# Kernel optimization log

Hardware: AMD Instinct MI355X
Metric: run time of the kernel (lower is better)

The kernel has to match this reference:

```python
import jax, jax.numpy as jnp
import numpy as np

N_POINTS = 131072
N_SEG = 16
C = 256
BN_EPS = 1e-5


def setup_inputs() -> dict:
    key = jax.random.key(0)
    ks = jax.random.split(key, 6)
    x = jax.random.normal(ks[0], (N_POINTS, C), jnp.float32)
    # Ragged segment end-offsets (cumulative counts), strictly increasing, last == N_POINTS.
    rng = np.random.default_rng(0)
    base = N_POINTS // N_SEG
    counts = base + rng.integers(-base // 32, base // 32, N_SEG)
    counts[-1] += N_POINTS - counts.sum()
    o = jnp.asarray(np.cumsum(counts), jnp.int32)
    s1 = 1.0 / np.sqrt(2 * C)  # linear1: Linear(2C -> C)
    s2 = 1.0 / np.sqrt(C)      # linear2: Linear(C -> C)
    W1 = jax.random.uniform(ks[1], (2 * C, C), jnp.float32, -s1, s1)
    b1 = jax.random.uniform(ks[2], (C,), jnp.float32, -s1, s1)
    W2 = jax.random.uniform(ks[3], (C, C), jnp.float32, -s2, s2)
    b2 = jax.random.uniform(ks[4], (C,), jnp.float32, -s2, s2)
    gamma = jnp.ones((C,), jnp.float32)
    beta = jnp.zeros((C,), jnp.float32)
    return {"x": x, "o": o, "W1": W1, "b1": b1, "W2": W2, "b2": b2,
            "gamma": gamma, "beta": beta}


def reference(x, o, W1, b1, W2, b2, gamma, beta):
    n, c = x.shape
    s = o.shape[0]
    # segment id per point from cumulative end-offsets
    seg_id = jnp.searchsorted(o, jnp.arange(n), side="right")  # [N]
    counts = jnp.concatenate([o[:1], o[1:] - o[:-1]])          # [S]
    # per-segment mean pooling (x_b.sum(0, True) / cnt)
    sums = jax.ops.segment_sum(x, seg_id, num_segments=s)      # [S, C]
    means = sums / counts[:, None].astype(x.dtype)
    # linear2: Linear(C, C) + ReLU on segment means
    y = jax.nn.relu(means @ W2 + b2)                           # [S, C]
    # broadcast-concat back to points, then linear1: Linear(2C, C)
    h = jnp.concatenate([x, y[seg_id]], axis=1) @ W1 + b1      # [N, C]
    # BatchNorm1d (training mode: batch statistics, biased variance) + ReLU
    mu = h.mean(axis=0)
    var = h.var(axis=0)
    out = jax.nn.relu((h - mu) * (gamma / jnp.sqrt(var + BN_EPS)) + beta)
    return out
```

## Files before the change

### kernel.cpp

```cpp
#include <hip/hip_runtime.h>
#include <hip/hip_bf16.h>
#include <stdint.h>

#define N_PTS 131072
#define NC 256
#define NSEG 16
#define BN_EPSF 1e-5f

typedef __attribute__((ext_vector_type(8))) short bf16x8;
typedef __attribute__((ext_vector_type(4))) float f32x4;

__device__ __forceinline__ unsigned short f2bf(float f) {
  union { float f; uint32_t u; } v; v.f = f;
  uint32_t u = v.u;
  uint32_t r = (u + 0x7fffu + ((u >> 16) & 1u)) >> 16;
  return (unsigned short)r;
}
__device__ __forceinline__ float bf2f(unsigned short h) {
  union { uint32_t u; float f; } v; v.u = ((uint32_t)h) << 16; return v.f;
}

__global__ void k_zero(float* __restrict__ p, int n) {
  int i = blockIdx.x * 256 + threadIdx.x;
  if (i < n) p[i] = 0.f;
}

__global__ __launch_bounds__(256) void k_segsum_convert(
    const float* __restrict__ x, const int* __restrict__ o,
    unsigned short* __restrict__ x_bf, float* __restrict__ seg_sums) {
  __shared__ int o_s[NSEG];
  int t = threadIdx.x;
  if (t < NSEG) o_s[t] = o[t];
  __syncthreads();
  int g = t >> 6, l = t & 63;
  int row0 = blockIdx.x * 128;
  int c0 = l * 4;
  int cur = 0;
  {
    int rf = row0 + g;
    while (o_s[cur] <= rf) ++cur;
  }
  float4 acc = {0.f, 0.f, 0.f, 0.f};
  const float4* xv = (const float4*)x;
  for (int i = 0; i < 32; ++i) {
    int r = row0 + g + i * 4;
    if (r >= o_s[cur]) {
      atomicAdd(&seg_sums[cur * NC + c0 + 0], acc.x);
      atomicAdd(&seg_sums[cur * NC + c0 + 1], acc.y);
      atomicAdd(&seg_sums[cur * NC + c0 + 2], acc.z);
      atomicAdd(&seg_sums[cur * NC + c0 + 3], acc.w);
      acc.x = acc.y = acc.z = acc.w = 0.f;
      do { ++cur; } while (o_s[cur] <= r);
    }
    float4 v = xv[r * 64 + l];
    ushort4 b;
    b.x = f2bf(v.x); b.y = f2bf(v.y); b.z = f2bf(v.z); b.w = f2bf(v.w);
    *(ushort4*)(x_bf + r * NC + c0) = b;
    acc.x += v.x; acc.y += v.y; acc.z += v.z; acc.w += v.w;
  }
  atomicAdd(&seg_sums[cur * NC + c0 + 0], acc.x);
  atomicAdd(&seg_sums[cur * NC + c0 + 1], acc.y);
  atomicAdd(&seg_sums[cur * NC + c0 + 2], acc.z);
  atomicAdd(&seg_sums[cur * NC + c0 + 3], acc.w);
}

__global__ void k_w1t(const float* __restrict__ W1, unsigned short* __restrict__ w1t) {
  int j = blockIdx.x, k = threadIdx.x;
  w1t[j * NC + k] = f2bf(W1[k * NC + j]);
}

__global__ __launch_bounds__(256) void k_seg_mlp(
    const int* __restrict__ o, const float* __restrict__ seg_sums,
    const float* __restrict__ W1, const float* __restrict__ b1,
    const float* __restrict__ W2, const float* __restrict__ b2,
    float* __restrict__ z) {
  __shared__ float mean_s[NC];
  __shared__ float y_s[NC];
  int b = blockIdx.x, j = threadIdx.x;
  int start = (b == 0) ? 0 : o[b - 1];
  float inv = 1.f / (float)(o[b] - start);
  mean_s[j] = seg_sums[b * NC + j] * inv;
  __syncthreads();
  float a = b2[j];
  for (int k = 0; k < NC; ++k) a += mean_s[k] * W2[k * NC + j];
  y_s[j] = fmaxf(a, 0.f);
  __syncthreads();
  float a2 = b1[j];
  for (int k = 0; k < NC; ++k) a2 += y_s[k] * W1[(NC + k) * NC + j];
  z[b * NC + j] = a2;
}

__global__ __launch_bounds__(256) void k_gemm(
    const unsigned short* __restrict__ x_bf, const unsigned short* __restrict__ w1t,
    const int* __restrict__ o, const float* __restrict__ z,
    unsigned short* __restrict__ h_bf,
    float* __restrict__ colsum, float* __restrict__ colsumsq) {
  __shared__ __align__(16) unsigned short lA[128 * 32];
  __shared__ __align__(16) unsigned short lB[128 * 32];
  __shared__ float s_sum[128];
  __shared__ float s_sq[128];
  __shared__ int o_s[NSEG];

  int t = threadIdx.x;
  int lane = t & 63, w = t >> 6;
  int wr = w >> 1, wc = w & 1;
  int bid = blockIdx.x;
  int ct = bid & 1, rt = bid >> 1;
  const int row0 = rt * 128, colT = ct * 128;

  if (t < 128) { s_sum[t] = 0.f; s_sq[t] = 0.f; }
  if (t < NSEG) o_s[t] = o[t];

  f32x4 acc[4][4] = {};

  for (int kt = 0; kt < 8; ++kt) {
    {
      int c = t;
      const unsigned short* ga = x_bf + (size_t)(row0 + (c >> 2)) * NC + kt * 32 + (c & 3) * 8;
      __builtin_amdgcn_global_load_lds(
          (const __attribute__((address_space(1))) void*)ga,
          (__attribute__((address_space(3))) void*)(lA + c * 8), 16, 0, 0);
      const unsigned short* gb = w1t + (size_t)(colT + (c >> 2)) * NC + kt * 32 + (c & 3) * 8;
      __builtin_amdgcn_global_load_lds(
          (const __attribute__((address_space(1))) void*)gb,
          (__attribute__((address_space(3))) void*)(lB + c * 8), 16, 0, 0);
      c = t + 256;
      ga = x_bf + (size_t)(row0 + (c >> 2)) * NC + kt * 32 + (c & 3) * 8;
      __builtin_amdgcn_global_load_lds(
          (const __attribute__((address_space(1))) void*)ga,
          (__attribute__((address_space(3))) void*)(lA + c * 8), 16, 0, 0);
      gb = w1t + (size_t)(colT + (c >> 2)) * NC + kt * 32 + (c & 3) * 8;
      __builtin_amdgcn_global_load_lds(
          (const __attribute__((address_space(1))) void*)gb,
          (__attribute__((address_space(3))) void*)(lB + c * 8), 16, 0, 0);
    }
    __syncthreads();
    bf16x8 af[4], bf[4];
#pragma unroll
    for (int m = 0; m < 4; ++m)
      af[m] = *(const bf16x8*)(lA + (wr * 64 + m * 16 + (lane & 15)) * 32 + (lane >> 4) * 8);
#pragma unroll
    for (int n = 0; n < 4; ++n)
      bf[n] = *(const bf16x8*)(lB + (wc * 64 + n * 16 + (lane & 15)) * 32 + (lane >> 4) * 8);
#pragma unroll
    for (int m = 0; m < 4; ++m)
#pragma unroll
      for (int n = 0; n < 4; ++n)
        acc[m][n] = __builtin_amdgcn_mfma_f32_16x16x32_bf16(af[m], bf[n], acc[m][n], 0, 0, 0);
    __syncthreads();
  }

  int s0 = 0;
  while (o_s[s0] <= row0) ++s0;
  int e0 = o_s[s0];
  int s1 = (s0 < NSEG - 1) ? s0 + 1 : s0;
  int cl = lane & 15, q = lane >> 4;
#pragma unroll
  for (int n = 0; n < 4; ++n) {
    int col = colT + wc * 64 + n * 16 + cl;
    float zA = z[s0 * NC + col], zB = z[s1 * NC + col];
    float ps = 0.f, pq = 0.f;
#pragma unroll
    for (int m = 0; m < 4; ++m) {
      int rbase = row0 + wr * 64 + m * 16 + q * 4;
#pragma unroll
      for (int r = 0; r < 4; ++r) {
        int row = rbase + r;
        float hv = acc[m][n][r] + ((row < e0) ? zA : zB);
        h_bf[(size_t)row * NC + col] = f2bf(hv);
        ps += hv; pq += hv * hv;
      }
    }
    ps += __shfl_xor(ps, 16, 64); ps += __shfl_xor(ps, 32, 64);
    pq += __shfl_xor(pq, 16, 64); pq += __shfl_xor(pq, 32, 64);
    if (q == 0) {
      atomicAdd(&s_sum[wc * 64 + n * 16 + cl], ps);
      atomicAdd(&s_sq[wc * 64 + n * 16 + cl], pq);
    }
  }
  __syncthreads();
  if (t < 128) {
    atomicAdd(&colsum[colT + t], s_sum[t]);
    atomicAdd(&colsumsq[colT + t], s_sq[t]);
  }
}

__global__ void k_bn_final(const float* __restrict__ colsum, const float* __restrict__ colsumsq,
                           const float* __restrict__ gamma, const float* __restrict__ beta,
                           float* __restrict__ scale, float* __restrict__ shift) {
  int t = threadIdx.x;
  float invN = 1.f / (float)N_PTS;
  float mu = colsum[t] * invN;
  float var = colsumsq[t] * invN - mu * mu;
  float sc = gamma[t] * rsqrtf(var + BN_EPSF);
  scale[t] = sc;
  shift[t] = beta[t] - mu * sc;
}

__global__ __launch_bounds__(256) void k_bn_apply(
    const unsigned short* __restrict__ h_bf, const float* __restrict__ scale,
    const float* __restrict__ shift, float* __restrict__ out) {
  __shared__ float s_sc[NC];
  __shared__ float s_sh[NC];
  int t = threadIdx.x;
  s_sc[t] = scale[t];
  s_sh[t] = shift[t];
  __syncthreads();
  size_t idx = (size_t)blockIdx.x * 256 + t;
  size_t l0 = idx * 8;
  int col = (int)(l0 & 255);
  uint4 hv = *(const uint4*)(h_bf + l0);
  float f0 = bf2f((unsigned short)(hv.x & 0xffffu));
  float f1 = bf2f((unsigned short)(hv.x >> 16));
  float f2 = bf2f((unsigned short)(hv.y & 0xffffu));
  float f3 = bf2f((unsigned short)(hv.y >> 16));
  float f4 = bf2f((unsigned short)(hv.z & 0xffffu));
  float f5 = bf2f((unsigned short)(hv.z >> 16));
  float f6 = bf2f((unsigned short)(hv.w & 0xffffu));
  float f7 = bf2f((unsigned short)(hv.w >> 16));
  float4 o0, o1;
  o0.x = fmaxf(f0 * s_sc[col + 0] + s_sh[col + 0], 0.f);
  o0.y = fmaxf(f1 * s_sc[col + 1] + s_sh[col + 1], 0.f);
  o0.z = fmaxf(f2 * s_sc[col + 2] + s_sh[col + 2], 0.f);
  o0.w = fmaxf(f3 * s_sc[col + 3] + s_sh[col + 3], 0.f);
  o1.x = fmaxf(f4 * s_sc[col + 4] + s_sh[col + 4], 0.f);
  o1.y = fmaxf(f5 * s_sc[col + 5] + s_sh[col + 5], 0.f);
  o1.z = fmaxf(f6 * s_sc[col + 6] + s_sh[col + 6], 0.f);
  o1.w = fmaxf(f7 * s_sc[col + 7] + s_sh[col + 7], 0.f);
  *(float4*)(out + l0) = o0;
  *(float4*)(out + l0 + 4) = o1;
}

extern "C" void kernel_launch(void* const* d_in, const int* in_sizes, int n_in,
                              void* d_out, int out_size, void* d_ws, size_t ws_size,
                              hipStream_t stream) {
  const float* x = (const float*)d_in[0];
  const int* o = (const int*)d_in[1];
  const float* W1 = (const float*)d_in[2];
  const float* b1 = (const float*)d_in[3];
  const float* W2 = (const float*)d_in[4];
  const float* b2 = (const float*)d_in[5];
  const float* gamma = (const float*)d_in[6];
  const float* beta = (const float*)d_in[7];
  float* out = (float*)d_out;

  char* ws = (char*)d_ws;
  unsigned short* x_bf = (unsigned short*)ws;
  unsigned short* h_bf = (unsigned short*)(ws + 67108864);
  char* base2 = ws + 134217728;
  float* seg_sums = (float*)(base2);
  float* colsum   = (float*)(base2 + 16384);
  float* colsumsq = (float*)(base2 + 17408);
  float* z        = (float*)(base2 + 18432);
  float* scale    = (float*)(base2 + 34816);
  float* shift    = (float*)(base2 + 35840);
  unsigned short* w1t = (unsigned short*)(base2 + 36864);

  k_zero<<<18, 256, 0, stream>>>(seg_sums, 4608);
  k_segsum_convert<<<1024, 256, 0, stream>>>(x, o, x_bf, seg_sums);
  k_w1t<<<256, 256, 0, stream>>>(W1, w1t);
  k_seg_mlp<<<16, 256, 0, stream>>>(o, seg_sums, W1, b1, W2, b2, z);
  k_gemm<<<2048, 256, 0, stream>>>(x_bf, w1t, o, z, h_bf, colsum, colsumsq);
  k_bn_final<<<1, 256, 0, stream>>>(colsum, colsumsq, gamma, beta, scale, shift);
  k_bn_apply<<<16384, 256, 0, stream>>>(h_bf, scale, shift, out);
}
```

Measured before the change: 380.4 us.

## Reduce segment sums in shared memory, tile W1 transpose, narrow bn_apply per thread

```diff
diff --git a/kernel.cpp b/kernel.cpp
--- a/kernel.cpp
+++ b/kernel.cpp
@@ -29,44 +29,65 @@
     const float* __restrict__ x, const int* __restrict__ o,
     unsigned short* __restrict__ x_bf, float* __restrict__ seg_sums) {
   __shared__ int o_s[NSEG];
+  __shared__ float s_acc[2][NC];
   int t = threadIdx.x;
   if (t < NSEG) o_s[t] = o[t];
+  s_acc[0][t] = 0.f;
+  s_acc[1][t] = 0.f;
   __syncthreads();
   int g = t >> 6, l = t & 63;
-  int row0 = blockIdx.x * 128;
+  int row0 = blockIdx.x * 64;
   int c0 = l * 4;
-  int cur = 0;
-  {
-    int rf = row0 + g;
-    while (o_s[cur] <= rf) ++cur;
-  }
-  float4 acc = {0.f, 0.f, 0.f, 0.f};
+  int s0 = 0;
+  while (o_s[s0] <= row0) ++s0;
+  int e0 = o_s[s0];
+  int s1 = (s0 < NSEG - 1) ? s0 + 1 : s0;
+  float4 accA = {0.f, 0.f, 0.f, 0.f}, accB = {0.f, 0.f, 0.f, 0.f};
   const float4* xv = (const float4*)x;
-  for (int i = 0; i < 32; ++i) {
+#pragma unroll
+  for (int i = 0; i < 16; ++i) {
     int r = row0 + g + i * 4;
-    if (r >= o_s[cur]) {
-      atomicAdd(&seg_sums[cur * NC + c0 + 0], acc.x);
-      atomicAdd(&seg_sums[cur * NC + c0 + 1], acc.y);
-      atomicAdd(&seg_sums[cur * NC + c0 + 2], acc.z);
-      atomicAdd(&seg_sums[cur * NC + c0 + 3], acc.w);
-      acc.x = acc.y = acc.z = acc.w = 0.f;
-      do { ++cur; } while (o_s[cur] <= r);
-    }
-    float4 v = xv[r * 64 + l];
+    float4 v = xv[(size_t)r * 64 + l];
     ushort4 b;
     b.x = f2bf(v.x); b.y = f2bf(v.y); b.z = f2bf(v.z); b.w = f2bf(v.w);
-    *(ushort4*)(x_bf + r * NC + c0) = b;
-    acc.x += v.x; acc.y += v.y; acc.z += v.z; acc.w += v.w;
-  }
-  atomicAdd(&seg_sums[cur * NC + c0 + 0], acc.x);
-  atomicAdd(&seg_sums[cur * NC + c0 + 1], acc.y);
-  atomicAdd(&seg_sums[cur * NC + c0 + 2], acc.z);
-  atomicAdd(&seg_sums[cur * NC + c0 + 3], acc.w);
-}
-
-__global__ void k_w1t(const float* __restrict__ W1, unsigned short* __restrict__ w1t) {
-  int j = blockIdx.x, k = threadIdx.x;
-  w1t[j * NC + k] = f2bf(W1[k * NC + j]);
+    *(ushort4*)(x_bf + (size_t)r * NC + c0) = b;
+    bool inA = (r < e0);
+    accA.x += inA ? v.x : 0.f; accB.x += inA ? 0.f : v.x;
+    accA.y += inA ? v.y : 0.f; accB.y += inA ? 0.f : v.y;
+    accA.z += inA ? v.z : 0.f; accB.z += inA ? 0.f : v.z;
+    accA.w += inA ? v.w : 0.f; accB.w += inA ? 0.f : v.w;
+  }
+  atomicAdd(&s_acc[0][c0 + 0], accA.x);
+  atomicAdd(&s_acc[0][c0 + 1], accA.y);
+  atomicAdd(&s_acc[0][c0 + 2], accA.z);
+  atomicAdd(&s_acc[0][c0 + 3], accA.w);
+  atomicAdd(&s_acc[1][c0 + 0], accB.x);
+  atomicAdd(&s_acc[1][c0 + 1], accB.y);
+  atomicAdd(&s_acc[1][c0 + 2], accB.z);
+  atomicAdd(&s_acc[1][c0 + 3], accB.w);
+  __syncthreads();
+  atomicAdd(&seg_sums[s0 * NC + t], s_acc[0][t]);
+  atomicAdd(&seg_sums[s1 * NC + t], s_acc[1][t]);
+}
+
+__global__ __launch_bounds__(256) void k_w1t(const float* __restrict__ W1,
+                                             unsigned short* __restrict__ w1t) {
+  __shared__ float tile[64][65];
+  int t = threadIdx.x;
+  int bx = blockIdx.x & 3, by = blockIdx.x >> 2;
+  int k0 = by * 64, j0 = bx * 64;
+  int r = t >> 6, c = t & 63;
+#pragma unroll
+  for (int i = 0; i < 16; ++i) {
+    int kk = r + i * 4;
+    tile[kk][c] = W1[(size_t)(k0 + kk) * NC + j0 + c];
+  }
+  __syncthreads();
+#pragma unroll
+  for (int i = 0; i < 16; ++i) {
+    int jj = r + i * 4;
+    w1t[(size_t)(j0 + jj) * NC + k0 + c] = f2bf(tile[c][jj]);
+  }
 }
 
 __global__ __launch_bounds__(256) void k_seg_mlp(
@@ -200,35 +221,23 @@
 __global__ __launch_bounds__(256) void k_bn_apply(
     const unsigned short* __restrict__ h_bf, const float* __restrict__ scale,
     const float* __restrict__ shift, float* __restrict__ out) {
-  __shared__ float s_sc[NC];
-  __shared__ float s_sh[NC];
-  int t = threadIdx.x;
-  s_sc[t] = scale[t];
-  s_sh[t] = shift[t];
-  __syncthreads();
+  int t = threadIdx.x;
   size_t idx = (size_t)blockIdx.x * 256 + t;
-  size_t l0 = idx * 8;
+  size_t l0 = idx * 4;
   int col = (int)(l0 & 255);
-  uint4 hv = *(const uint4*)(h_bf + l0);
+  uint2 hv = *(const uint2*)(h_bf + l0);
+  float4 sc = *(const float4*)(scale + col);
+  float4 sh = *(const float4*)(shift + col);
   float f0 = bf2f((unsigned short)(hv.x & 0xffffu));
   float f1 = bf2f((unsigned short)(hv.x >> 16));
   float f2 = bf2f((unsigned short)(hv.y & 0xffffu));
   float f3 = bf2f((unsigned short)(hv.y >> 16));
-  float f4 = bf2f((unsigned short)(hv.z & 0xffffu));
-  float f5 = bf2f((unsigned short)(hv.z >> 16));
-  float f6 = bf2f((unsigned short)(hv.w & 0xffffu));
-  float f7 = bf2f((unsigned short)(hv.w >> 16));
-  float4 o0, o1;
-  o0.x = fmaxf(f0 * s_sc[col + 0] + s_sh[col + 0], 0.f);
-  o0.y = fmaxf(f1 * s_sc[col + 1] + s_sh[col + 1], 0.f);
-  o0.z = fmaxf(f2 * s_sc[col + 2] + s_sh[col + 2], 0.f);
-  o0.w = fmaxf(f3 * s_sc[col + 3] + s_sh[col + 3], 0.f);
-  o1.x = fmaxf(f4 * s_sc[col + 4] + s_sh[col + 4], 0.f);
-  o1.y = fmaxf(f5 * s_sc[col + 5] + s_sh[col + 5], 0.f);
-  o1.z = fmaxf(f6 * s_sc[col + 6] + s_sh[col + 6], 0.f);
-  o1.w = fmaxf(f7 * s_sc[col + 7] + s_sh[col + 7], 0.f);
+  float4 o0;
+  o0.x = fmaxf(f0 * sc.x + sh.x, 0.f);
+  o0.y = fmaxf(f1 * sc.y + sh.y, 0.f);
+  o0.z = fmaxf(f2 * sc.z + sh.z, 0.f);
+  o0.w = fmaxf(f3 * sc.w + sh.w, 0.f);
   *(float4*)(out + l0) = o0;
-  *(float4*)(out + l0 + 4) = o1;
 }
 
 extern "C" void kernel_launch(void* const* d_in, const int* in_sizes, int n_in,
@@ -257,10 +266,10 @@
   unsigned short* w1t = (unsigned short*)(base2 + 36864);
 
   k_zero<<<18, 256, 0, stream>>>(seg_sums, 4608);
-  k_segsum_convert<<<1024, 256, 0, stream>>>(x, o, x_bf, seg_sums);
-  k_w1t<<<256, 256, 0, stream>>>(W1, w1t);
+  k_segsum_convert<<<2048, 256, 0, stream>>>(x, o, x_bf, seg_sums);
+  k_w1t<<<16, 256, 0, stream>>>(W1, w1t);
   k_seg_mlp<<<16, 256, 0, stream>>>(o, seg_sums, W1, b1, W2, b2, z);
   k_gemm<<<2048, 256, 0, stream>>>(x_bf, w1t, o, z, h_bf, colsum, colsumsq);
   k_bn_final<<<1, 256, 0, stream>>>(colsum, colsumsq, gamma, beta, scale, shift);
-  k_bn_apply<<<16384, 256, 0, stream>>>(h_bf, scale, shift, out);
-}
+  k_bn_apply<<<32768, 256, 0, stream>>>(h_bf, scale, shift, out);
+}
```

After: 350.0 us. -8.0%, faster.
